# Kernel optimization log

Measured on AMD Instinct MI355X. Metric: run time of the kernel, lower is better.

Reference implementation:

```python
import jax, jax.numpy as jnp
import numpy as np

N_NODES = 100000
IN_DIM = 64
OUT_DIM = 64
N_EDGES = 1250000


def setup_inputs() -> dict:
    key = jax.random.key(0)
    k1, k2, k3, k4 = jax.random.split(key, 4)
    x = jax.random.normal(k1, (N_NODES, IN_DIM), dtype=jnp.float32)
    edge_index = jax.random.randint(k2, (2, N_EDGES), 0, N_NODES, dtype=jnp.int32)
    # Linear weights stored as [in, out] so y = x @ W (equivalent to torch x @ W.T)
    s = 1.0 / np.sqrt(IN_DIM)
    W1 = jax.random.uniform(k3, (IN_DIM, OUT_DIM), dtype=jnp.float32, minval=-s, maxval=s)
    W2 = jax.random.uniform(k4, (IN_DIM, OUT_DIM), dtype=jnp.float32, minval=-s, maxval=s)
    return {"x": x, "edge_index": edge_index, "W1": W1, "W2": W2}


def reference(x, edge_index, W1, W2):
    # self part: [N, out]
    self_part = x @ W1
    # transform-then-gather is mathematically identical to gather-then-transform
    # (linear map commutes with row gather) and cheaper when E > N.
    msgs = (x @ W2)[edge_index[0]]            # [E, out]
    neighbor_part = jax.ops.segment_sum(msgs, edge_index[1], num_segments=x.shape[0])
    return jax.nn.relu(self_part + neighbor_part)
```

## Files before the change

kernel.cpp:

```cpp
#include <hip/hip_runtime.h>

#define N_NODES 100000
#define N_EDGES 1250000
#define DIM 64

#define B_SHIFT 7
#define BUCKET_NODES 128
#define NBUCKETS ((N_NODES + BUCKET_NODES - 1) / BUCKET_NODES)
#define CAP 2560
#define CHUNK 4096
#define NBLK_EDGE ((N_EDGES + CHUNK - 1) / CHUNK)
#define GEMM_BLOCKS 512
#define SG_THREADS 512

typedef __attribute__((ext_vector_type(8))) short short8;
typedef __attribute__((ext_vector_type(4))) float f32x4;

static __host__ __device__ inline size_t align256(size_t x) { return (x + 255) & ~(size_t)255; }

__device__ inline float bf16_to_f32(unsigned short u) {
  return __uint_as_float(((unsigned)u) << 16);
}
__device__ inline unsigned short f32_to_bf16(float f) {
  unsigned u = __float_as_uint(f);
  u += 0x7FFFu + ((u >> 16) & 1u);
  return (unsigned short)(u >> 16);
}

__global__ __launch_bounds__(256) void fused_gemm_partition(
    const float* __restrict__ x,
    const float* __restrict__ W1,
    const float* __restrict__ W2,
    float* __restrict__ y1,
    unsigned short* __restrict__ y2b,
    const int* __restrict__ ei,
    int* __restrict__ gcursor,
    unsigned* __restrict__ pairs,
    int nTiles) {
  __shared__ int h[NBUCKETS];
  __shared__ int gbase[NBUCKETS];

  if (blockIdx.x < NBLK_EDGE) {
    const int nE = N_EDGES;
    for (int i = threadIdx.x; i < NBUCKETS; i += 256) h[i] = 0;
    __syncthreads();
    int base = blockIdx.x * CHUNK;
    int end = min(base + CHUNK, nE);
    for (int e = base + (int)threadIdx.x; e < end; e += 256)
      atomicAdd(&h[ei[nE + e] >> B_SHIFT], 1);
    __syncthreads();
    for (int i = threadIdx.x; i < NBUCKETS; i += 256) {
      int c = h[i];
      gbase[i] = c ? atomicAdd(&gcursor[i], c) : 0;
      h[i] = 0;
    }
    __syncthreads();
    for (int e = base + (int)threadIdx.x; e < end; e += 256) {
      int dst = ei[nE + e];
      int src = ei[e];
      int b = dst >> B_SHIFT;
      int pos = gbase[b] + atomicAdd(&h[b], 1);
      if (pos < CAP)
        pairs[b * CAP + pos] = (unsigned)src | ((unsigned)(dst & (BUCKET_NODES - 1)) << 17);
    }
  } else {
    int lane = threadIdx.x & 63;
    int wave = ((blockIdx.x - NBLK_EDGE) * 256 + (int)threadIdx.x) >> 6;
    int nWaves = GEMM_BLOCKS * 4;
    int m = lane & 15;
    int q = lane >> 4;

    short8 wf[2][2][4];
#pragma unroll
    for (int w = 0; w < 2; ++w) {
      const float* W = w ? W2 : W1;
#pragma unroll
      for (int kh = 0; kh < 2; ++kh)
#pragma unroll
        for (int nt = 0; nt < 4; ++nt) {
          short8 f;
#pragma unroll
          for (int j = 0; j < 8; ++j) {
            int k = kh * 32 + q * 8 + j;
            f[j] = (short)f32_to_bf16(W[k * DIM + nt * 16 + m]);
          }
          wf[w][kh][nt] = f;
        }
    }

    for (int t = wave; t < nTiles; t += nWaves) {
      int rowBase = t * 16;
      const float* xr = x + (size_t)(rowBase + m) * DIM + q * 8;

      short8 af[2];
#pragma unroll
      for (int kh = 0; kh < 2; ++kh) {
        float4 u0 = *(const float4*)(xr + kh * 32);
        float4 u1 = *(const float4*)(xr + kh * 32 + 4);
        short8 f;
        f[0] = (short)f32_to_bf16(u0.x);
        f[1] = (short)f32_to_bf16(u0.y);
        f[2] = (short)f32_to_bf16(u0.z);
        f[3] = (short)f32_to_bf16(u0.w);
        f[4] = (short)f32_to_bf16(u1.x);
        f[5] = (short)f32_to_bf16(u1.y);
        f[6] = (short)f32_to_bf16(u1.z);
        f[7] = (short)f32_to_bf16(u1.w);
        af[kh] = f;
      }

      {
        f32x4 acc[4];
#pragma unroll
        for (int nt = 0; nt < 4; ++nt) {
          acc[nt] = (f32x4){0.f, 0.f, 0.f, 0.f};
          acc[nt] = __builtin_amdgcn_mfma_f32_16x16x32_bf16(af[0], wf[0][0][nt], acc[nt], 0, 0, 0);
          acc[nt] = __builtin_amdgcn_mfma_f32_16x16x32_bf16(af[1], wf[0][1][nt], acc[nt], 0, 0, 0);
        }
#pragma unroll
        for (int nt = 0; nt < 4; ++nt)
#pragma unroll
          for (int r = 0; r < 4; ++r)
            y1[(size_t)(rowBase + q * 4 + r) * DIM + nt * 16 + m] = acc[nt][r];
      }
      {
        f32x4 acc[4];
#pragma unroll
        for (int nt = 0; nt < 4; ++nt) {
          acc[nt] = (f32x4){0.f, 0.f, 0.f, 0.f};
          acc[nt] = __builtin_amdgcn_mfma_f32_16x16x32_bf16(af[0], wf[1][0][nt], acc[nt], 0, 0, 0);
          acc[nt] = __builtin_amdgcn_mfma_f32_16x16x32_bf16(af[1], wf[1][1][nt], acc[nt], 0, 0, 0);
        }
#pragma unroll
        for (int nt = 0; nt < 4; ++nt)
#pragma unroll
          for (int r = 0; r < 4; ++r)
            y2b[(size_t)(rowBase + q * 4 + r) * DIM + nt * 16 + m] = f32_to_bf16(acc[nt][r]);
      }
    }
  }
}

__global__ __launch_bounds__(SG_THREADS) void sort_gather(
    const unsigned* __restrict__ pairs,
    const int* __restrict__ gcursor,
    const unsigned short* __restrict__ y2b,
    float* __restrict__ out,
    int nNodesTotal) {
  __shared__ unsigned buf[CAP];
  __shared__ unsigned sorted[CAP];
  __shared__ int cnt[BUCKET_NODES];
  __shared__ int scn[BUCKET_NODES];
  __shared__ int cur[BUCKET_NODES];

  int b = blockIdx.x;
  int n = min(gcursor[b], CAP);
  int tid = threadIdx.x;
  const unsigned* pb = pairs + (size_t)b * CAP;

  if (tid < BUCKET_NODES) cnt[tid] = 0;
  __syncthreads();
  for (int i = tid; i < n; i += SG_THREADS) {
    unsigned w = pb[i];
    buf[i] = w;
    atomicAdd(&cnt[(w >> 17) & 127], 1);
  }
  __syncthreads();

  int v = 0;
  if (tid < BUCKET_NODES) { v = cnt[tid]; scn[tid] = v; }
  __syncthreads();
#pragma unroll
  for (int off = 1; off < BUCKET_NODES; off <<= 1) {
    int t = 0;
    if (tid < BUCKET_NODES && tid >= off) t = scn[tid - off];
    __syncthreads();
    if (tid < BUCKET_NODES) scn[tid] += t;
    __syncthreads();
  }
  if (tid < BUCKET_NODES) cur[tid] = scn[tid] - v;
  __syncthreads();

  for (int i = tid; i < n; i += SG_THREADS) {
    unsigned w = buf[i];
    int l = (int)((w >> 17) & 127);
    int p = atomicAdd(&cur[l], 1);
    sorted[p] = w & 0x1FFFFu;
  }
  __syncthreads();

  int lane = tid & 63;
  int wv = tid >> 6;
  int c = lane & 31;
  int hh = lane >> 5;
  const ushort2* y2v = (const ushort2*)y2b;
  int nodeBase = b << B_SHIFT;
  int numNodes = min(BUCKET_NODES, nNodesTotal - nodeBase);

  for (int ln = wv; ln < numNodes; ln += (SG_THREADS / 64)) {
    int deg = cnt[ln];
    int begin = scn[ln] - deg;
    int end = begin + deg;

    float ax0 = 0.f, ay0 = 0.f, ax1 = 0.f, ay1 = 0.f;
    float bx0 = 0.f, by0 = 0.f, bx1 = 0.f, by1 = 0.f;
    int e = begin;
    for (; e + 7 < end; e += 8) {
      int s0 = (int)sorted[e + hh];
      int s1 = (int)sorted[e + 2 + hh];
      int s2 = (int)sorted[e + 4 + hh];
      int s3 = (int)sorted[e + 6 + hh];
      ushort2 u0 = y2v[(size_t)s0 * 32 + c];
      ushort2 u1 = y2v[(size_t)s1 * 32 + c];
      ushort2 u2 = y2v[(size_t)s2 * 32 + c];
      ushort2 u3 = y2v[(size_t)s3 * 32 + c];
      ax0 += bf16_to_f32(u0.x); ay0 += bf16_to_f32(u0.y);
      ax1 += bf16_to_f32(u1.x); ay1 += bf16_to_f32(u1.y);
      bx0 += bf16_to_f32(u2.x); by0 += bf16_to_f32(u2.y);
      bx1 += bf16_to_f32(u3.x); by1 += bf16_to_f32(u3.y);
    }
    for (; e + 3 < end; e += 4) {
      int s0 = (int)sorted[e + hh];
      int s1 = (int)sorted[e + 2 + hh];
      ushort2 u0 = y2v[(size_t)s0 * 32 + c];
      ushort2 u1 = y2v[(size_t)s1 * 32 + c];
      ax0 += bf16_to_f32(u0.x); ay0 += bf16_to_f32(u0.y);
      ax1 += bf16_to_f32(u1.x); ay1 += bf16_to_f32(u1.y);
    }
    for (; e < end; e += 2) {
      int ee = e + hh;
      if (ee < end) {
        int s = (int)sorted[ee];
        ushort2 u = y2v[(size_t)s * 32 + c];
        ax0 += bf16_to_f32(u.x); ay0 += bf16_to_f32(u.y);
      }
    }

    float sx = (ax0 + ax1) + (bx0 + bx1);
    float sy = (ay0 + ay1) + (by0 + by1);
    sx += __shfl_xor(sx, 32, 64);
    sy += __shfl_xor(sy, 32, 64);

    if (lane < 32) {
      float2* ov = (float2*)out;
      size_t idx = (size_t)(nodeBase + ln) * 32 + lane;
      float2 o = ov[idx];
      o.x = fmaxf(o.x + sx, 0.0f);
      o.y = fmaxf(o.y + sy, 0.0f);
      ov[idx] = o;
    }
  }
}

__global__ __launch_bounds__(256) void gemm_simple(
    const float* __restrict__ x, const float* __restrict__ W1, const float* __restrict__ W2,
    float* __restrict__ y1, unsigned short* __restrict__ y2b, int n) {
  int row = blockIdx.x * blockDim.x + threadIdx.x;
  if (row >= n) return;
  float xv[DIM];
  const float4* xr = (const float4*)(x + (size_t)row * DIM);
#pragma unroll
  for (int i = 0; i < DIM / 4; ++i) {
    float4 t = xr[i];
    xv[4 * i] = t.x; xv[4 * i + 1] = t.y; xv[4 * i + 2] = t.z; xv[4 * i + 3] = t.w;
  }
#pragma unroll
  for (int m = 0; m < 2; ++m) {
    const float* W = (m == 0) ? W1 : W2;
#pragma unroll
    for (int cc = 0; cc < DIM; cc += 16) {
      float acc[16];
#pragma unroll
      for (int c2 = 0; c2 < 16; ++c2) acc[c2] = 0.0f;
      for (int k = 0; k < DIM; ++k) {
        float xk = xv[k];
        const float* wr = W + k * DIM + cc;
#pragma unroll
        for (int c2 = 0; c2 < 16; ++c2) acc[c2] = fmaf(xk, wr[c2], acc[c2]);
      }
      if (m == 0) {
        for (int c2 = 0; c2 < 16; ++c2) y1[(size_t)row * DIM + cc + c2] = acc[c2];
      } else {
        for (int c2 = 0; c2 < 16; ++c2) y2b[(size_t)row * DIM + cc + c2] = f32_to_bf16(acc[c2]);
      }
    }
  }
}

__global__ __launch_bounds__(256) void scatter_add(const int* __restrict__ ei,
                                                   const unsigned short* __restrict__ y2b,
                                                   float* __restrict__ out, int nE) {
  int gid = blockIdx.x * blockDim.x + threadIdx.x;
  int edge = gid >> 6;
  int lane = threadIdx.x & 63;
  if (edge >= nE) return;
  int src = __builtin_amdgcn_readfirstlane(ei[edge]);
  int dst = __builtin_amdgcn_readfirstlane(ei[nE + edge]);
  atomicAdd(&out[(size_t)dst * DIM + lane], bf16_to_f32(y2b[(size_t)src * DIM + lane]));
}

__global__ __launch_bounds__(256) void relu_inplace(float* __restrict__ out, int n4) {
  int i = blockIdx.x * blockDim.x + threadIdx.x;
  if (i >= n4) return;
  float4* p = (float4*)out;
  float4 v = p[i];
  v.x = fmaxf(v.x, 0.0f);
  v.y = fmaxf(v.y, 0.0f);
  v.z = fmaxf(v.z, 0.0f);
  v.w = fmaxf(v.w, 0.0f);
  p[i] = v;
}

extern "C" void kernel_launch(void* const* d_in, const int* in_sizes, int n_in,
                              void* d_out, int out_size, void* d_ws, size_t ws_size,
                              hipStream_t stream) {
  const float* x  = (const float*)d_in[0];
  const int*   ei = (const int*)d_in[1];
  const float* W1 = (const float*)d_in[2];
  const float* W2 = (const float*)d_in[3];
  float* out = (float*)d_out;

  char* ws = (char*)d_ws;
  size_t off = 0;
  unsigned short* y2b = (unsigned short*)(ws + off); off += align256((size_t)N_NODES * DIM * sizeof(unsigned short));
  int* gcursor = (int*)(ws + off);                   off += align256((size_t)NBUCKETS * sizeof(int));
  unsigned* pairs = (unsigned*)(ws + off);           off += align256((size_t)NBUCKETS * CAP * sizeof(unsigned));
  size_t required = off;

  if (ws_size >= required) {
    hipMemsetAsync(gcursor, 0, (size_t)NBUCKETS * sizeof(int), stream);
    fused_gemm_partition<<<NBLK_EDGE + GEMM_BLOCKS, 256, 0, stream>>>(
        x, W1, W2, out, y2b, ei, gcursor, pairs, N_NODES / 16);
    sort_gather<<<NBUCKETS, SG_THREADS, 0, stream>>>(pairs, gcursor, y2b, out, N_NODES);
  } else {
    {
      int blocks = (N_NODES + 255) / 256;
      gemm_simple<<<blocks, 256, 0, stream>>>(x, W1, W2, out, y2b, N_NODES);
    }
    {
      long long threads = (long long)N_EDGES * 64;
      int blocks = (int)((threads + 255) / 256);
      scatter_add<<<blocks, 256, 0, stream>>>(ei, y2b, out, N_EDGES);
    }
    {
      int n4 = N_NODES * DIM / 4;
      int blocks = (n4 + 255) / 256;
      relu_inplace<<<blocks, 256, 0, stream>>>(out, n4);
    }
  }
}
```

Before: 155.9 us.

## Split fused partition/GEMM kernel and store self term as bf16 scratch

Splits the fused edge-partition and GEMM kernel into two separate launches. The self-projection x@W1 is now stored in bf16 in a workspace buffer instead of fp32 in the output, and sort_gather writes the output once rather than doing a read-modify-write. Chunk size and GEMM block count are also retuned. This cuts traffic on the self term but adds a launch, loses the overlap between partitioning and GEMM, and rounds the self term to bf16.

Result: slower. 159.1 us (+2.1%).

```diff
diff --git a/kernel.cpp b/kernel.cpp
--- a/kernel.cpp
+++ b/kernel.cpp
@@ -8,9 +8,9 @@
 #define BUCKET_NODES 128
 #define NBUCKETS ((N_NODES + BUCKET_NODES - 1) / BUCKET_NODES)
 #define CAP 2560
-#define CHUNK 4096
+#define CHUNK 2048
 #define NBLK_EDGE ((N_EDGES + CHUNK - 1) / CHUNK)
-#define GEMM_BLOCKS 512
+#define GEMM_BLOCKS 1024
 #define SG_THREADS 512
 
 typedef __attribute__((ext_vector_type(8))) short short8;
@@ -27,116 +27,104 @@
   return (unsigned short)(u >> 16);
 }
 
-__global__ __launch_bounds__(256) void fused_gemm_partition(
+__global__ __launch_bounds__(256) void partition_edges(
+    const int* __restrict__ ei,
+    int* __restrict__ gcursor,
+    unsigned* __restrict__ pairs) {
+  __shared__ int h[NBUCKETS];
+  __shared__ int gbase[NBUCKETS];
+  const int nE = N_EDGES;
+
+  for (int i = threadIdx.x; i < NBUCKETS; i += 256) h[i] = 0;
+  __syncthreads();
+  int base = blockIdx.x * CHUNK;
+  int end = min(base + CHUNK, nE);
+  for (int e = base + (int)threadIdx.x; e < end; e += 256)
+    atomicAdd(&h[ei[nE + e] >> B_SHIFT], 1);
+  __syncthreads();
+  for (int i = threadIdx.x; i < NBUCKETS; i += 256) {
+    int c = h[i];
+    gbase[i] = c ? atomicAdd(&gcursor[i], c) : 0;
+    h[i] = 0;
+  }
+  __syncthreads();
+  for (int e = base + (int)threadIdx.x; e < end; e += 256) {
+    int dst = ei[nE + e];
+    int src = ei[e];
+    int b = dst >> B_SHIFT;
+    int pos = gbase[b] + atomicAdd(&h[b], 1);
+    if (pos < CAP)
+      pairs[b * CAP + pos] = (unsigned)src | ((unsigned)(dst & (BUCKET_NODES - 1)) << 17);
+  }
+}
+
+__global__ __launch_bounds__(256) void gemm_mfma(
     const float* __restrict__ x,
     const float* __restrict__ W1,
     const float* __restrict__ W2,
-    float* __restrict__ y1,
+    unsigned short* __restrict__ y1b,
     unsigned short* __restrict__ y2b,
-    const int* __restrict__ ei,
-    int* __restrict__ gcursor,
-    unsigned* __restrict__ pairs,
     int nTiles) {
-  __shared__ int h[NBUCKETS];
-  __shared__ int gbase[NBUCKETS];
-
-  if (blockIdx.x < NBLK_EDGE) {
-    const int nE = N_EDGES;
-    for (int i = threadIdx.x; i < NBUCKETS; i += 256) h[i] = 0;
-    __syncthreads();
-    int base = blockIdx.x * CHUNK;
-    int end = min(base + CHUNK, nE);
-    for (int e = base + (int)threadIdx.x; e < end; e += 256)
-      atomicAdd(&h[ei[nE + e] >> B_SHIFT], 1);
-    __syncthreads();
-    for (int i = threadIdx.x; i < NBUCKETS; i += 256) {
-      int c = h[i];
-      gbase[i] = c ? atomicAdd(&gcursor[i], c) : 0;
-      h[i] = 0;
-    }
-    __syncthreads();
-    for (int e = base + (int)threadIdx.x; e < end; e += 256) {
-      int dst = ei[nE + e];
-      int src = ei[e];
-      int b = dst >> B_SHIFT;
-      int pos = gbase[b] + atomicAdd(&h[b], 1);
-      if (pos < CAP)
-        pairs[b * CAP + pos] = (unsigned)src | ((unsigned)(dst & (BUCKET_NODES - 1)) << 17);
-    }
-  } else {
-    int lane = threadIdx.x & 63;
-    int wave = ((blockIdx.x - NBLK_EDGE) * 256 + (int)threadIdx.x) >> 6;
-    int nWaves = GEMM_BLOCKS * 4;
-    int m = lane & 15;
-    int q = lane >> 4;
-
-    short8 wf[2][2][4];
+  int lane = threadIdx.x & 63;
+  int wave = (blockIdx.x * 256 + (int)threadIdx.x) >> 6;
+  int nWaves = GEMM_BLOCKS * 4;
+  int m = lane & 15;
+  int q = lane >> 4;
+
+  short8 wf[2][2][4];
+#pragma unroll
+  for (int w = 0; w < 2; ++w) {
+    const float* W = w ? W2 : W1;
+#pragma unroll
+    for (int kh = 0; kh < 2; ++kh)
+#pragma unroll
+      for (int nt = 0; nt < 4; ++nt) {
+        short8 f;
+#pragma unroll
+        for (int j = 0; j < 8; ++j) {
+          int k = kh * 32 + q * 8 + j;
+          f[j] = (short)f32_to_bf16(W[k * DIM + nt * 16 + m]);
+        }
+        wf[w][kh][nt] = f;
+      }
+  }
+
+  for (int t = wave; t < nTiles; t += nWaves) {
+    int rowBase = t * 16;
+    const float* xr = x + (size_t)(rowBase + m) * DIM + q * 8;
+
+    short8 af[2];
+#pragma unroll
+    for (int kh = 0; kh < 2; ++kh) {
+      float4 u0 = *(const float4*)(xr + kh * 32);
+      float4 u1 = *(const float4*)(xr + kh * 32 + 4);
+      short8 f;
+      f[0] = (short)f32_to_bf16(u0.x);
+      f[1] = (short)f32_to_bf16(u0.y);
+      f[2] = (short)f32_to_bf16(u0.z);
+      f[3] = (short)f32_to_bf16(u0.w);
+      f[4] = (short)f32_to_bf16(u1.x);
+      f[5] = (short)f32_to_bf16(u1.y);
+      f[6] = (short)f32_to_bf16(u1.z);
+      f[7] = (short)f32_to_bf16(u1.w);
+      af[kh] = f;
+    }
+
 #pragma unroll
     for (int w = 0; w < 2; ++w) {
-      const float* W = w ? W2 : W1;
-#pragma unroll
-      for (int kh = 0; kh < 2; ++kh)
-#pragma unroll
-        for (int nt = 0; nt < 4; ++nt) {
-          short8 f;
-#pragma unroll
-          for (int j = 0; j < 8; ++j) {
-            int k = kh * 32 + q * 8 + j;
-            f[j] = (short)f32_to_bf16(W[k * DIM + nt * 16 + m]);
-          }
-          wf[w][kh][nt] = f;
-        }
-    }
-
-    for (int t = wave; t < nTiles; t += nWaves) {
-      int rowBase = t * 16;
-      const float* xr = x + (size_t)(rowBase + m) * DIM + q * 8;
-
-      short8 af[2];
-#pragma unroll
-      for (int kh = 0; kh < 2; ++kh) {
-        float4 u0 = *(const float4*)(xr + kh * 32);
-        float4 u1 = *(const float4*)(xr + kh * 32 + 4);
-        short8 f;
-        f[0] = (short)f32_to_bf16(u0.x);
-        f[1] = (short)f32_to_bf16(u0.y);
-        f[2] = (short)f32_to_bf16(u0.z);
-        f[3] = (short)f32_to_bf16(u0.w);
-        f[4] = (short)f32_to_bf16(u1.x);
-        f[5] = (short)f32_to_bf16(u1.y);
-        f[6] = (short)f32_to_bf16(u1.z);
-        f[7] = (short)f32_to_bf16(u1.w);
-        af[kh] = f;
-      }
-
-      {
-        f32x4 acc[4];
-#pragma unroll
-        for (int nt = 0; nt < 4; ++nt) {
-          acc[nt] = (f32x4){0.f, 0.f, 0.f, 0.f};
-          acc[nt] = __builtin_amdgcn_mfma_f32_16x16x32_bf16(af[0], wf[0][0][nt], acc[nt], 0, 0, 0);
-          acc[nt] = __builtin_amdgcn_mfma_f32_16x16x32_bf16(af[1], wf[0][1][nt], acc[nt], 0, 0, 0);
-        }
-#pragma unroll
-        for (int nt = 0; nt < 4; ++nt)
-#pragma unroll
-          for (int r = 0; r < 4; ++r)
-            y1[(size_t)(rowBase + q * 4 + r) * DIM + nt * 16 + m] = acc[nt][r];
-      }
-      {
-        f32x4 acc[4];
-#pragma unroll
-        for (int nt = 0; nt < 4; ++nt) {
-          acc[nt] = (f32x4){0.f, 0.f, 0.f, 0.f};
-          acc[nt] = __builtin_amdgcn_mfma_f32_16x16x32_bf16(af[0], wf[1][0][nt], acc[nt], 0, 0, 0);
-          acc[nt] = __builtin_amdgcn_mfma_f32_16x16x32_bf16(af[1], wf[1][1][nt], acc[nt], 0, 0, 0);
-        }
-#pragma unroll
-        for (int nt = 0; nt < 4; ++nt)
-#pragma unroll
-          for (int r = 0; r < 4; ++r)
-            y2b[(size_t)(rowBase + q * 4 + r) * DIM + nt * 16 + m] = f32_to_bf16(acc[nt][r]);
-      }
+      unsigned short* Y = w ? y2b : y1b;
+      f32x4 acc[4];
+#pragma unroll
+      for (int nt = 0; nt < 4; ++nt) {
+        acc[nt] = (f32x4){0.f, 0.f, 0.f, 0.f};
+        acc[nt] = __builtin_amdgcn_mfma_f32_16x16x32_bf16(af[0], wf[w][0][nt], acc[nt], 0, 0, 0);
+        acc[nt] = __builtin_amdgcn_mfma_f32_16x16x32_bf16(af[1], wf[w][1][nt], acc[nt], 0, 0, 0);
+      }
+#pragma unroll
+      for (int nt = 0; nt < 4; ++nt)
+#pragma unroll
+        for (int r = 0; r < 4; ++r)
+          Y[(size_t)(rowBase + q * 4 + r) * DIM + nt * 16 + m] = f32_to_bf16(acc[nt][r]);
     }
   }
 }
@@ -144,6 +132,7 @@
 __global__ __launch_bounds__(SG_THREADS) void sort_gather(
     const unsigned* __restrict__ pairs,
     const int* __restrict__ gcursor,
+    const unsigned short* __restrict__ y1b,
     const unsigned short* __restrict__ y2b,
     float* __restrict__ out,
     int nNodesTotal) {
@@ -194,6 +183,7 @@
   int c = lane & 31;
   int hh = lane >> 5;
   const ushort2* y2v = (const ushort2*)y2b;
+  const ushort2* y1v = (const ushort2*)y1b;
   int nodeBase = b << B_SHIFT;
   int numNodes = min(BUCKET_NODES, nNodesTotal - nodeBase);
 
@@ -242,12 +232,13 @@
     sy += __shfl_xor(sy, 32, 64);
 
     if (lane < 32) {
+      int node = nodeBase + ln;
+      ushort2 s1v = y1v[(size_t)node * 32 + c];
       float2* ov = (float2*)out;
-      size_t idx = (size_t)(nodeBase + ln) * 32 + lane;
-      float2 o = ov[idx];
-      o.x = fmaxf(o.x + sx, 0.0f);
-      o.y = fmaxf(o.y + sy, 0.0f);
-      ov[idx] = o;
+      float2 o;
+      o.x = fmaxf(bf16_to_f32(s1v.x) + sx, 0.0f);
+      o.y = fmaxf(bf16_to_f32(s1v.y) + sy, 0.0f);
+      ov[(size_t)node * 32 + c] = o;
     }
   }
 }
@@ -323,15 +314,16 @@
   char* ws = (char*)d_ws;
   size_t off = 0;
   unsigned short* y2b = (unsigned short*)(ws + off); off += align256((size_t)N_NODES * DIM * sizeof(unsigned short));
+  unsigned short* y1b = (unsigned short*)(ws + off); off += align256((size_t)N_NODES * DIM * sizeof(unsigned short));
   int* gcursor = (int*)(ws + off);                   off += align256((size_t)NBUCKETS * sizeof(int));
   unsigned* pairs = (unsigned*)(ws + off);           off += align256((size_t)NBUCKETS * CAP * sizeof(unsigned));
   size_t required = off;
 
   if (ws_size >= required) {
     hipMemsetAsync(gcursor, 0, (size_t)NBUCKETS * sizeof(int), stream);
-    fused_gemm_partition<<<NBLK_EDGE + GEMM_BLOCKS, 256, 0, stream>>>(
-        x, W1, W2, out, y2b, ei, gcursor, pairs, N_NODES / 16);
-    sort_gather<<<NBUCKETS, SG_THREADS, 0, stream>>>(pairs, gcursor, y2b, out, N_NODES);
+    partition_edges<<<NBLK_EDGE, 256, 0, stream>>>(ei, gcursor, pairs);
+    gemm_mfma<<<GEMM_BLOCKS, 256, 0, stream>>>(x, W1, W2, y1b, y2b, N_NODES / 16);
+    sort_gather<<<NBUCKETS, SG_THREADS, 0, stream>>>(pairs, gcursor, y1b, y2b, out, N_NODES);
   } else {
     {
       int blocks = (N_NODES + 255) / 256;
```
